# Performance work log

Hardware: AMD Instinct MI355X
Metric: run time of the kernel (lower is better)

The kernel has to match this reference:

```python
import jax, jax.numpy as jnp
import numpy as np

B, T, W, L, H, TW = 2, 4096, 2048, 2048, 8, 4
HD = L // H  # head dim for block-diagonal gate projections


def setup_inputs() -> dict:
    key = jax.random.key(0)
    ks = jax.random.split(key, 16)
    inv_sqrt_w = 1.0 / np.sqrt(W)
    inv_sqrt_l = 1.0 / np.sqrt(L)
    inv_sqrt_hd = 1.0 / np.sqrt(HD)
    return {
        "x": jax.random.normal(ks[0], (B, T, W), dtype=jnp.float32),
        "segment_pos": jnp.tile(jnp.arange(T, dtype=jnp.int32), (B, 1)),
        # linear_y, linear_x: width -> lru_width
        "w_y": jax.random.normal(ks[1], (W, L), dtype=jnp.float32) * inv_sqrt_w,
        "b_y": jnp.zeros((L,), dtype=jnp.float32),
        "w_x": jax.random.normal(ks[2], (W, L), dtype=jnp.float32) * inv_sqrt_w,
        "b_x": jnp.zeros((L,), dtype=jnp.float32),
        # linear_out: lru_width -> width
        "w_out": jax.random.normal(ks[3], (L, W), dtype=jnp.float32) * inv_sqrt_l,
        "b_out": jnp.zeros((W,), dtype=jnp.float32),
        # depthwise causal temporal conv, kernel [TW, L]
        "conv_w": jax.random.normal(ks[4], (TW, L), dtype=jnp.float32) / np.sqrt(TW),
        "conv_b": jnp.zeros((L,), dtype=jnp.float32),
        # RG-LRU: a_param and two block-diagonal gate projections
        "a_param": jax.random.uniform(ks[5], (L,), dtype=jnp.float32, minval=-2.0, maxval=1.0),
        "igate_w": jax.random.normal(ks[6], (H, HD, HD), dtype=jnp.float32) * inv_sqrt_hd,
        "igate_b": jnp.zeros((H, HD), dtype=jnp.float32),
        "agate_w": jax.random.normal(ks[7], (H, HD, HD), dtype=jnp.float32) * inv_sqrt_hd,
        "agate_b": jnp.zeros((H, HD), dtype=jnp.float32),
    }


def _block_diag_linear(u, w, b):
    # u: [B,T,L] -> [B,T,H,HD] blockwise projected -> [B,T,L]
    uh = u.reshape(u.shape[0], u.shape[1], H, HD)
    y = jnp.einsum("bthd,hde->bthe", uh, w) + b
    return y.reshape(u.shape)


def _forward(x, segment_pos, w_y, b_y, w_x, b_x, w_out, b_out,
             conv_w, conv_b, a_param, igate_w, igate_b, agate_w, agate_b):
    # gate branch: linear_y + tanh-approx GELU
    y = jax.nn.gelu(jnp.einsum("btw,wl->btl", x, w_y) + b_y, approximate=True)
    # recurrent branch: linear_x
    xb = jnp.einsum("btw,wl->btl", x, w_x) + b_x
    # causal depthwise temporal conv (width TW), zero history before t=0
    x_pad = jnp.pad(xb, ((0, 0), (TW - 1, 0), (0, 0)))
    conv = conv_b + sum(conv_w[j] * x_pad[:, j:j + T] for j in range(TW))
    # RG-LRU gates
    gate_x = jax.nn.sigmoid(_block_diag_linear(conv, igate_w, igate_b))
    gate_a = jax.nn.sigmoid(_block_diag_linear(conv, agate_w, agate_b))
    log_a = -8.0 * gate_a * jax.nn.softplus(a_param)  # [B,T,L]
    a = jnp.exp(log_a)
    reset = (segment_pos == 0)[..., None]  # [B,T,1]
    multiplier = jnp.sqrt(1.0 - jnp.exp(2.0 * log_a))
    multiplier = jnp.where(reset, 1.0, multiplier)
    normed = conv * gate_x * multiplier
    a_masked = jnp.where(reset, 0.0, a)
    # diagonal linear recurrence: h_t = a_t * h_{t-1} + normed_t
    def step(h, inp):
        a_t, x_t = inp
        h = a_t * h + x_t
        return h, h
    h0 = jnp.zeros((x.shape[0], L), dtype=x.dtype)
    _, hs = jax.lax.scan(step, h0, (a_masked.transpose(1, 0, 2), normed.transpose(1, 0, 2)))
    hs = hs.transpose(1, 0, 2)  # [B,T,L]
    # elementwise gate then output projection
    return jnp.einsum("btl,lw->btw", hs * y, w_out) + b_out


def reference(x, segment_pos, w_y, b_y, w_x, b_x, w_out, b_out,
              conv_w, conv_b, a_param, igate_w, igate_b, agate_w, agate_b):
    return _forward(x, segment_pos, w_y, b_y, w_x, b_x, w_out, b_out,
                    conv_w, conv_b, a_param, igate_w, igate_b, agate_w, agate_b)
```

## Files before the change

### kernel.cpp

```cpp
#include <hip/hip_runtime.h>
#include <cstdint>
#include <math.h>

typedef _Float16 f16;
typedef f16 f16x8 __attribute__((ext_vector_type(8)));
typedef f16 f16x4 __attribute__((ext_vector_type(4)));
typedef float f32x4 __attribute__((ext_vector_type(4)));

#define BATCH 2
#define TSEQ 4096
#define WID 2048
#define LRU 2048
#define NHEAD 8
#define HDIM 256
#define MTOT (BATCH * TSEQ)
#define CT 128
#define NC (TSEQ / CT)

__device__ __forceinline__ void gl2lds16(const f16* g, f16* l) {
  __builtin_amdgcn_global_load_lds(
      (__attribute__((address_space(1))) uint32_t*)(uintptr_t)g,
      (__attribute__((address_space(3))) uint32_t*)(uint32_t)(uintptr_t)l,
      16, 0, 0);
}

__device__ __forceinline__ float sigmoidf_(float x) { return 1.f / (1.f + expf(-x)); }
__device__ __forceinline__ float f16bits_to_f(uint32_t b) {
  return (float)__builtin_bit_cast(f16, (uint16_t)b);
}

__global__ void prep_kernel(const float* __restrict__ x, f16* __restrict__ Xh,
                            const float* __restrict__ w_y, const float* __restrict__ w_x,
                            const float* __restrict__ w_out,
                            f16* __restrict__ wyT, f16* __restrict__ wxT, f16* __restrict__ woutT,
                            const float* __restrict__ ig, const float* __restrict__ ag,
                            f16* __restrict__ igT, f16* __restrict__ agT) {
  __shared__ float tile[32][33];
  const int bid = blockIdx.x, t = threadIdx.x;
  if (bid < 16384) {
    int i = bid * 256 + t;
    float4 v = ((const float4*)x)[i];
    f16x4 o = { (f16)v.x, (f16)v.y, (f16)v.z, (f16)v.w };
    ((f16x4*)Xh)[i] = o;
    return;
  }
  const int tx = t & 31, ty = t >> 5;
  const float* ib; f16* ob; int R, C, c0, r0;
  if (bid < 28672) {
    int idx = bid - 16384;
    int z = idx >> 12, tl = idx & 4095;
    ib = z == 0 ? w_y : (z == 1 ? w_x : w_out);
    ob = z == 0 ? wyT : (z == 1 ? wxT : woutT);
    R = 2048; C = 2048;
    c0 = (tl & 63) * 32; r0 = (tl >> 6) * 32;
  } else {
    int idx = bid - 28672;
    int z = idx >> 6, tl = idx & 63;
    ib = (z < 8 ? ig : ag) + (long long)(z & 7) * HDIM * HDIM;
    ob = (z < 8 ? igT : agT) + (long long)(z & 7) * HDIM * HDIM;
    R = HDIM; C = HDIM;
    c0 = (tl & 7) * 32; r0 = (tl >> 3) * 32;
  }
#pragma unroll
  for (int i = 0; i < 32; i += 8)
    tile[ty + i][tx] = ib[(long long)(r0 + ty + i) * C + c0 + tx];
  __syncthreads();
#pragma unroll
  for (int i = 0; i < 32; i += 8)
    ob[(long long)(c0 + ty + i) * R + r0 + tx] = (f16)tile[tx][ty + i];
}

__global__ __launch_bounds__(256, 2) void gemm_dual(
    const f16* __restrict__ A, const f16* __restrict__ B1T, const f16* __restrict__ B2T,
    const float* __restrict__ b1, const float* __restrict__ b2,
    f16* __restrict__ Y, f16* __restrict__ X2, int M, int N, int K) {
  __shared__ __align__(16) f16 As[3][128 * 32];
  __shared__ __align__(16) f16 B1s[3][128 * 32];
  __shared__ __align__(16) f16 B2s[3][128 * 32];
  const int m0 = blockIdx.x * 128, n0 = blockIdx.y * 128;
  const int t = threadIdx.x;
  const int lane = t & 63, wave = t >> 6;
  const int wr = (wave >> 1) * 64, wc = (wave & 1) * 64;
  const int l15 = lane & 15, quad = lane >> 4;
  const int srow = t >> 2;
  const int scol = ((t & 3) ^ ((srow >> 1) & 3)) * 8;
  const int sl = (quad ^ ((l15 >> 1) & 3)) * 8;

  const f16* Ag = A + (long long)(m0 + srow) * K + scol;
  const f16* B1g = B1T + (long long)(n0 + srow) * K + scol;
  const f16* B2g = B2T + (long long)(n0 + srow) * K + scol;
  const long long h64 = (long long)64 * K;

  auto STAGE = [&](int tt, int bb) {
    const f16* a = Ag + tt * 32;
    const f16* p1 = B1g + tt * 32;
    const f16* p2 = B2g + tt * 32;
    gl2lds16(a, &As[bb][t * 8]);    gl2lds16(a + h64, &As[bb][64 * 32 + t * 8]);
    gl2lds16(p1, &B1s[bb][t * 8]);  gl2lds16(p1 + h64, &B1s[bb][64 * 32 + t * 8]);
    gl2lds16(p2, &B2s[bb][t * 8]);  gl2lds16(p2 + h64, &B2s[bb][64 * 32 + t * 8]);
  };

  f32x4 c1[4][4] = {};
  f32x4 c2[4][4] = {};
  const int NT = K >> 5;
  STAGE(0, 0); STAGE(1, 1);
  asm volatile("s_waitcnt vmcnt(6)" ::: "memory");
  __builtin_amdgcn_s_barrier();
  __builtin_amdgcn_sched_barrier(0);
  int bufc = 0, bufs = 2;
  for (int tt = 0; tt < NT; ++tt) {
    if (tt + 2 < NT) STAGE(tt + 2, bufs);
    f16x8 af[4], b1f[4], b2f[4];
#pragma unroll
    for (int i = 0; i < 4; ++i)
      af[i] = *(const f16x8*)&As[bufc][(wr + i * 16 + l15) * 32 + sl];
#pragma unroll
    for (int j = 0; j < 4; ++j) {
      b1f[j] = *(const f16x8*)&B1s[bufc][(wc + j * 16 + l15) * 32 + sl];
      b2f[j] = *(const f16x8*)&B2s[bufc][(wc + j * 16 + l15) * 32 + sl];
    }
    __builtin_amdgcn_s_setprio(1);
#pragma unroll
    for (int i = 0; i < 4; ++i)
#pragma unroll
      for (int j = 0; j < 4; ++j) {
        c1[i][j] = __builtin_amdgcn_mfma_f32_16x16x32_f16(af[i], b1f[j], c1[i][j], 0, 0, 0);
        c2[i][j] = __builtin_amdgcn_mfma_f32_16x16x32_f16(af[i], b2f[j], c2[i][j], 0, 0, 0);
      }
    __builtin_amdgcn_s_setprio(0);
    if (tt + 1 < NT) {
      if (tt + 2 < NT) { asm volatile("s_waitcnt vmcnt(6)" ::: "memory"); }
      else             { asm volatile("s_waitcnt vmcnt(0)" ::: "memory"); }
      __builtin_amdgcn_s_barrier();
      __builtin_amdgcn_sched_barrier(0);
    }
    bufc = (bufc + 1 == 3) ? 0 : bufc + 1;
    bufs = (bufs + 1 == 3) ? 0 : bufs + 1;
  }
#pragma unroll
  for (int i = 0; i < 4; ++i) {
#pragma unroll
    for (int j = 0; j < 4; ++j) {
      const int col = n0 + wc + j * 16 + l15;
      const float b1v = b1[col], b2v = b2[col];
      const int row0 = m0 + wr + i * 16 + quad * 4;
#pragma unroll
      for (int r = 0; r < 4; ++r) {
        long long off = (long long)(row0 + r) * N + col;
        float v = c1[i][j][r] + b1v;
        float u = v + 0.044715f * v * v * v;
        float g = 0.5f * v * (1.f + tanhf(0.7978845608028654f * u));
        Y[off] = (f16)g;
        X2[off] = (f16)(c2[i][j][r] + b2v);
      }
    }
  }
}

__global__ __launch_bounds__(256, 2) void gemm_bt(
    const f16* __restrict__ A, const f16* __restrict__ BT, const float* __restrict__ bias,
    float* __restrict__ Cf, int M, int N, int K) {
  __shared__ __align__(16) f16 As[3][128 * 32];
  __shared__ __align__(16) f16 Bs[3][128 * 32];
  const int m0 = blockIdx.x * 128, n0 = blockIdx.y * 128;
  const int t = threadIdx.x;
  const int lane = t & 63, wave = t >> 6;
  const int wr = (wave >> 1) * 64, wc = (wave & 1) * 64;
  const int l15 = lane & 15, quad = lane >> 4;
  const int srow = t >> 2;
  const int scol = ((t & 3) ^ ((srow >> 1) & 3)) * 8;
  const int sl = (quad ^ ((l15 >> 1) & 3)) * 8;

  const f16* Ag = A + (long long)(m0 + srow) * K + scol;
  const f16* Bg = BT + (long long)(n0 + srow) * K + scol;
  const long long h64 = (long long)64 * K;

  auto STAGE = [&](int tt, int bb) {
    const f16* a = Ag + tt * 32;
    const f16* p = Bg + tt * 32;
    gl2lds16(a, &As[bb][t * 8]); gl2lds16(a + h64, &As[bb][64 * 32 + t * 8]);
    gl2lds16(p, &Bs[bb][t * 8]); gl2lds16(p + h64, &Bs[bb][64 * 32 + t * 8]);
  };

  f32x4 acc[4][4] = {};
  const int NT = K >> 5;
  STAGE(0, 0); STAGE(1, 1);
  asm volatile("s_waitcnt vmcnt(4)" ::: "memory");
  __builtin_amdgcn_s_barrier();
  __builtin_amdgcn_sched_barrier(0);
  int bufc = 0, bufs = 2;
  for (int tt = 0; tt < NT; ++tt) {
    if (tt + 2 < NT) STAGE(tt + 2, bufs);
    f16x8 af[4], bf[4];
#pragma unroll
    for (int i = 0; i < 4; ++i)
      af[i] = *(const f16x8*)&As[bufc][(wr + i * 16 + l15) * 32 + sl];
#pragma unroll
    for (int j = 0; j < 4; ++j)
      bf[j] = *(const f16x8*)&Bs[bufc][(wc + j * 16 + l15) * 32 + sl];
    __builtin_amdgcn_s_setprio(1);
#pragma unroll
    for (int i = 0; i < 4; ++i)
#pragma unroll
      for (int j = 0; j < 4; ++j)
        acc[i][j] = __builtin_amdgcn_mfma_f32_16x16x32_f16(af[i], bf[j], acc[i][j], 0, 0, 0);
    __builtin_amdgcn_s_setprio(0);
    if (tt + 1 < NT) {
      if (tt + 2 < NT) { asm volatile("s_waitcnt vmcnt(4)" ::: "memory"); }
      else             { asm volatile("s_waitcnt vmcnt(0)" ::: "memory"); }
      __builtin_amdgcn_s_barrier();
      __builtin_amdgcn_sched_barrier(0);
    }
    bufc = (bufc + 1 == 3) ? 0 : bufc + 1;
    bufs = (bufs + 1 == 3) ? 0 : bufs + 1;
  }
#pragma unroll
  for (int i = 0; i < 4; ++i) {
#pragma unroll
    for (int j = 0; j < 4; ++j) {
      const int col = n0 + wc + j * 16 + l15;
      const float bv = bias[col];
      const int row0 = m0 + wr + i * 16 + quad * 4;
#pragma unroll
      for (int r = 0; r < 4; ++r)
        Cf[(long long)(row0 + r) * N + col] = acc[i][j][r] + bv;
    }
  }
}

__global__ __launch_bounds__(256, 2) void gates_fused(
    const f16* __restrict__ XBh, const float* __restrict__ cw, const float* __restrict__ cb,
    const f16* __restrict__ BiT, const f16* __restrict__ BaT,
    const float* __restrict__ ib, const float* __restrict__ ab,
    const float* __restrict__ a_param, const int* __restrict__ segpos,
    uint32_t* __restrict__ AN, float* __restrict__ Ac, float* __restrict__ Hc) {
  __shared__ __align__(16) f16 As[128 * 256];
  __shared__ __align__(16) f16 Bi[128 * 32];
  __shared__ __align__(16) f16 Ba[128 * 32];
  const int m0 = blockIdx.x * 128;
  const int h = blockIdx.y >> 1;
  const int half = blockIdx.y & 1;
  const int ncol0 = h * HDIM + half * 128;
  const int t = threadIdx.x;
  const int lane = t & 63, wave = t >> 6;
  const int wr = (wave >> 1) * 64, wc = (wave & 1) * 64;
  const int l15 = lane & 15, quad = lane >> 4;

#pragma unroll 4
  for (int it = 0; it < 16; ++it) {
    int idx = it * 256 + t;
    int r = idx >> 5, kc = idx & 31;
    int m = m0 + r, tpos = m & (TSEQ - 1);
    int colbase = h * HDIM + kc * 8;
    float acc[8];
    {
      float4 c0 = *(const float4*)&cb[colbase];
      float4 c1 = *(const float4*)&cb[colbase + 4];
      acc[0] = c0.x; acc[1] = c0.y; acc[2] = c0.z; acc[3] = c0.w;
      acc[4] = c1.x; acc[5] = c1.y; acc[6] = c1.z; acc[7] = c1.w;
    }
#pragma unroll
    for (int d = 0; d < 4; ++d) {
      if (tpos >= d) {
        f16x8 xv = *(const f16x8*)&XBh[(long long)(m - d) * LRU + colbase];
        float4 w0 = *(const float4*)&cw[(3 - d) * LRU + colbase];
        float4 w1 = *(const float4*)&cw[(3 - d) * LRU + colbase + 4];
        acc[0] += w0.x * (float)xv[0]; acc[1] += w0.y * (float)xv[1];
        acc[2] += w0.z * (float)xv[2]; acc[3] += w0.w * (float)xv[3];
        acc[4] += w1.x * (float)xv[4]; acc[5] += w1.y * (float)xv[5];
        acc[6] += w1.z * (float)xv[6]; acc[7] += w1.w * (float)xv[7];
      }
    }
    f16x8 o;
#pragma unroll
    for (int k = 0; k < 8; ++k) o[k] = (f16)acc[k];
    int gs = (kc & ~7) | ((kc ^ r) & 7);
    *(f16x8*)&As[r * 256 + gs * 8] = o;
  }
  __syncthreads();

  const int srow = t >> 2, scol = (t & 3) * 8;
  const f16* Big = BiT + (long long)(ncol0 + srow) * HDIM + scol;
  const f16* Bag = BaT + (long long)(ncol0 + srow) * HDIM + scol;
  f32x4 ci[4][4] = {};
  f32x4 ca[4][4] = {};
  for (int k0 = 0; k0 < HDIM; k0 += 32) {
    gl2lds16(Big, &Bi[t * 8]); gl2lds16(Big + 64 * HDIM, &Bi[64 * 32 + t * 8]);
    gl2lds16(Bag, &Ba[t * 8]); gl2lds16(Bag + 64 * HDIM, &Ba[64 * 32 + t * 8]);
    Big += 32; Bag += 32;
    __syncthreads();
    f16x8 af[4], bif[4], baf[4];
#pragma unroll
    for (int i = 0; i < 4; ++i) {
      int row = wr + i * 16 + l15;
      int g = (k0 >> 3) + quad;
      int gsw = (g & ~7) | ((g ^ row) & 7);
      af[i] = *(const f16x8*)&As[row * 256 + gsw * 8];
    }
#pragma unroll
    for (int j = 0; j < 4; ++j) {
      bif[j] = *(const f16x8*)&Bi[(wc + j * 16 + l15) * 32 + quad * 8];
      baf[j] = *(const f16x8*)&Ba[(wc + j * 16 + l15) * 32 + quad * 8];
    }
#pragma unroll
    for (int i = 0; i < 4; ++i)
#pragma unroll
      for (int j = 0; j < 4; ++j) {
        ci[i][j] = __builtin_amdgcn_mfma_f32_16x16x32_f16(af[i], bif[j], ci[i][j], 0, 0, 0);
        ca[i][j] = __builtin_amdgcn_mfma_f32_16x16x32_f16(af[i], baf[j], ca[i][j], 0, 0, 0);
      }
    __syncthreads();
  }

  const int mb = m0 >> 12;
  const int cch = (m0 & (TSEQ - 1)) >> 7;
  float Aw[4], hw[4];
#pragma unroll
  for (int j = 0; j < 4; ++j) {
    const int cl = wc + j * 16 + l15;
    const int col = ncol0 + cl;
    const float ibv = ib[col], abv = ab[col];
    const float sp = log1pf(expf(a_param[col]));
    float A4[4], h4[4];
#pragma unroll
    for (int i = 0; i < 4; ++i) {
      float Aseg = 1.f, hseg = 0.f;
#pragma unroll
      for (int r = 0; r < 4; ++r) {
        const int rowL = wr + i * 16 + quad * 4 + r;
        const int row = m0 + rowL;
        float gx = sigmoidf_(ci[i][j][r] + ibv);
        float ga = sigmoidf_(ca[i][j][r] + abv);
        float la = -8.f * ga * sp;
        bool rs = (segpos[row] == 0);
        float a = rs ? 0.f : expf(la);
        uint32_t afx = __float2uint_rn(a * 65536.f);
        if (afx > 65535u) afx = 65535u;
        float aq = (float)afx * (1.f / 65536.f);
        int cfull = half * 128 + cl;
        int g = cfull >> 3, e = cfull & 7;
        int gsw = (g & ~7) | ((g ^ rowL) & 7);
        float cv = (float)As[rowL * 256 + gsw * 8 + e];
        float mult = rs ? 1.f : sqrtf(fmaxf(1.f - aq * aq, 0.f));
        f16 nh = (f16)(cv * gx * mult);
        AN[(long long)row * LRU + col] =
            afx | ((uint32_t)__builtin_bit_cast(uint16_t, nh) << 16);
        float xq = (float)nh;
        hseg = aq * hseg + xq;
        Aseg *= aq;
      }
      A4[i] = Aseg; h4[i] = hseg;
    }
#pragma unroll
    for (int i = 0; i < 4; ++i) {
      float A = A4[i], hv = h4[i];
#pragma unroll
      for (int d = 1; d <= 2; d <<= 1) {
        int src = quad >= d ? lane - 16 * d : lane;
        float Ap = __shfl(A, src);
        float hp = __shfl(hv, src);
        if (quad >= d) { hv = A * hp + hv; A = Ap * A; }
      }
      A4[i] = __shfl(A, 48 + l15);
      h4[i] = __shfl(hv, 48 + l15);
    }
    float Awv = 1.f, hwv = 0.f;
#pragma unroll
    for (int i = 0; i < 4; ++i) { hwv = A4[i] * hwv + h4[i]; Awv *= A4[i]; }
    Aw[j] = Awv; hw[j] = hwv;
  }
  float* carry = (float*)Bi;
  __syncthreads();
  if (wr == 0 && quad == 0) {
#pragma unroll
    for (int j = 0; j < 4; ++j) {
      int cl = wc + j * 16 + l15;
      carry[cl * 2] = Aw[j]; carry[cl * 2 + 1] = hw[j];
    }
  }
  __syncthreads();
  if (wr == 64 && quad == 0) {
#pragma unroll
    for (int j = 0; j < 4; ++j) {
      int cl = wc + j * 16 + l15;
      float At = carry[cl * 2], ht = carry[cl * 2 + 1];
      float A = At * Aw[j];
      float hv = Aw[j] * ht + hw[j];
      int o = (mb * NC + cch) * LRU + ncol0 + cl;
      Ac[o] = A; Hc[o] = hv;
    }
  }
}

__global__ void scan23_kernel(const uint32_t* __restrict__ AN,
                              const float* __restrict__ Ac, const float* __restrict__ Hc,
                              const f16* __restrict__ Yh, f16* __restrict__ G) {
  int l = blockIdx.x * 256 + threadIdx.x;
  int c = blockIdx.y, b = blockIdx.z;
  float hv = 0.f;
  for (int cc = 0; cc < c; ++cc) {
    int o = (b * NC + cc) * LRU + l;
    hv = Ac[o] * hv + Hc[o];
  }
  long long base = ((long long)b * TSEQ + (long long)c * CT) * LRU + l;
#pragma unroll 4
  for (int s = 0; s < CT; ++s) {
    long long o = base + (long long)s * LRU;
    uint32_t p = AN[o];
    float a = (float)(p & 0xFFFFu) * (1.f / 65536.f);
    float x = f16bits_to_f(p >> 16);
    hv = a * hv + x;
    G[o] = (f16)(hv * (float)Yh[o]);
  }
}

extern "C" void kernel_launch(void* const* d_in, const int* in_sizes, int n_in,
                              void* d_out, int out_size, void* d_ws, size_t ws_size,
                              hipStream_t stream) {
  (void)in_sizes; (void)n_in; (void)out_size; (void)ws_size;
  const float* x          = (const float*)d_in[0];
  const int*   segment_pos= (const int*)d_in[1];
  const float* w_y        = (const float*)d_in[2];
  const float* b_y        = (const float*)d_in[3];
  const float* w_x        = (const float*)d_in[4];
  const float* b_x        = (const float*)d_in[5];
  const float* w_out      = (const float*)d_in[6];
  const float* b_out      = (const float*)d_in[7];
  const float* conv_w     = (const float*)d_in[8];
  const float* conv_b     = (const float*)d_in[9];
  const float* a_param    = (const float*)d_in[10];
  const float* igate_w    = (const float*)d_in[11];
  const float* igate_b    = (const float*)d_in[12];
  const float* agate_w    = (const float*)d_in[13];
  const float* agate_b    = (const float*)d_in[14];
  float* out = (float*)d_out;

  char* base = (char*)d_ws;
  size_t off = 0;
  auto alloc = [&](size_t nbytes) -> void* {
    void* p = base + off;
    off = (off + nbytes + 255) & ~(size_t)255;
    return p;
  };
  f16*     Xh    = (f16*)alloc((size_t)MTOT * LRU * 2);
  f16*     Yh    = (f16*)alloc((size_t)MTOT * LRU * 2);
  f16*     XBh   = (f16*)alloc((size_t)MTOT * LRU * 2);
  uint32_t* AN   = (uint32_t*)alloc((size_t)MTOT * LRU * 4);
  f16*     wyT   = (f16*)alloc((size_t)WID * LRU * 2);
  f16*     wxT   = (f16*)alloc((size_t)WID * LRU * 2);
  f16*     woutT = (f16*)alloc((size_t)LRU * WID * 2);
  f16*     igwT  = (f16*)alloc((size_t)NHEAD * HDIM * HDIM * 2);
  f16*     agwT  = (f16*)alloc((size_t)NHEAD * HDIM * HDIM * 2);
  float*   Ac    = (float*)alloc((size_t)BATCH * NC * LRU * 4);
  float*   Hc    = (float*)alloc((size_t)BATCH * NC * LRU * 4);
  f16*     G     = Xh;

  prep_kernel<<<29696, 256, 0, stream>>>(x, Xh, w_y, w_x, w_out, wyT, wxT, woutT,
                                         igate_w, agate_w, igwT, agwT);
  gemm_dual<<<dim3(MTOT / 128, LRU / 128), 256, 0, stream>>>(
      Xh, wyT, wxT, b_y, b_x, Yh, XBh, MTOT, LRU, WID);
  gates_fused<<<dim3(MTOT / 128, 2 * NHEAD), 256, 0, stream>>>(
      XBh, conv_w, conv_b, igwT, agwT, igate_b, agate_b, a_param, segment_pos, AN, Ac, Hc);
  scan23_kernel<<<dim3(LRU / 256, NC, BATCH), 256, 0, stream>>>(AN, Ac, Hc, Yh, G);
  gemm_bt<<<dim3(MTOT / 128, WID / 128), 256, 0, stream>>>(G, woutT, b_out, out, MTOT, WID, LRU);
}
```

Baseline: 558.2 us.

## Replace 128x128 GEMMs with templated 256x256 tile GEMM using split-phase pipeline

Replaces the dual-output GEMM and the output GEMM with one templated 256x256-tile kernel run on 512 threads, with 8 waves each computing 128x64. The main loop is split into two MFMA phases, with LDS fragment loads and global-to-LDS staging of A and B interleaved between extra barriers. The larger tile is meant to raise arithmetic intensity and cut global traffic per FLOP. The cost is that the fused gate/x GEMM becomes two launches that each reread X, and the extra barriers add synchronisation. LDS use is 96KB per block, which may limit occupancy below the requested 2 blocks per CU.

```diff
diff --git a/kernel.cpp b/kernel.cpp
--- a/kernel.cpp
+++ b/kernel.cpp
@@ -70,160 +70,110 @@
     ob[(long long)(c0 + ty + i) * R + r0 + tx] = (f16)tile[tx][ty + i];
 }
 
-__global__ __launch_bounds__(256, 2) void gemm_dual(
-    const f16* __restrict__ A, const f16* __restrict__ B1T, const f16* __restrict__ B2T,
-    const float* __restrict__ b1, const float* __restrict__ b2,
-    f16* __restrict__ Y, f16* __restrict__ X2, int M, int N, int K) {
-  __shared__ __align__(16) f16 As[3][128 * 32];
-  __shared__ __align__(16) f16 B1s[3][128 * 32];
-  __shared__ __align__(16) f16 B2s[3][128 * 32];
-  const int m0 = blockIdx.x * 128, n0 = blockIdx.y * 128;
+template <int MODE>
+__global__ __launch_bounds__(512, 2) void gemm_256(
+    const f16* __restrict__ A, const f16* __restrict__ BT,
+    const float* __restrict__ bias, void* __restrict__ Cout,
+    int M, int N, int K) {
+  __shared__ __align__(16) f16 As[3][256 * 32];
+  __shared__ __align__(16) f16 Bs[3][256 * 32];
+  const int m0 = blockIdx.x * 256, n0 = blockIdx.y * 256;
   const int t = threadIdx.x;
   const int lane = t & 63, wave = t >> 6;
-  const int wr = (wave >> 1) * 64, wc = (wave & 1) * 64;
+  const int wr = (wave >> 2) * 128;
+  const int wc = (wave & 3) * 64;
   const int l15 = lane & 15, quad = lane >> 4;
   const int srow = t >> 2;
-  const int scol = ((t & 3) ^ ((srow >> 1) & 3)) * 8;
+  const int sg = ((t & 3) ^ ((srow >> 1) & 3)) * 8;
   const int sl = (quad ^ ((l15 >> 1) & 3)) * 8;
 
-  const f16* Ag = A + (long long)(m0 + srow) * K + scol;
-  const f16* B1g = B1T + (long long)(n0 + srow) * K + scol;
-  const f16* B2g = B2T + (long long)(n0 + srow) * K + scol;
-  const long long h64 = (long long)64 * K;
-
-  auto STAGE = [&](int tt, int bb) {
+  const f16* Ag = A + (long long)(m0 + srow) * K + sg;
+  const f16* Bg = BT + (long long)(n0 + srow) * K + sg;
+  const long long h128 = (long long)128 * K;
+
+  auto STAGE_A = [&](int tt, int bb) {
     const f16* a = Ag + tt * 32;
-    const f16* p1 = B1g + tt * 32;
-    const f16* p2 = B2g + tt * 32;
-    gl2lds16(a, &As[bb][t * 8]);    gl2lds16(a + h64, &As[bb][64 * 32 + t * 8]);
-    gl2lds16(p1, &B1s[bb][t * 8]);  gl2lds16(p1 + h64, &B1s[bb][64 * 32 + t * 8]);
-    gl2lds16(p2, &B2s[bb][t * 8]);  gl2lds16(p2 + h64, &B2s[bb][64 * 32 + t * 8]);
+    gl2lds16(a, &As[bb][t * 8]);
+    gl2lds16(a + h128, &As[bb][128 * 32 + t * 8]);
   };
-
-  f32x4 c1[4][4] = {};
-  f32x4 c2[4][4] = {};
+  auto STAGE_B = [&](int tt, int bb) {
+    const f16* b = Bg + tt * 32;
+    gl2lds16(b, &Bs[bb][t * 8]);
+    gl2lds16(b + h128, &Bs[bb][128 * 32 + t * 8]);
+  };
+
+  f32x4 c[8][4] = {};
   const int NT = K >> 5;
-  STAGE(0, 0); STAGE(1, 1);
-  asm volatile("s_waitcnt vmcnt(6)" ::: "memory");
-  __builtin_amdgcn_s_barrier();
-  __builtin_amdgcn_sched_barrier(0);
-  int bufc = 0, bufs = 2;
-  for (int tt = 0; tt < NT; ++tt) {
-    if (tt + 2 < NT) STAGE(tt + 2, bufs);
-    f16x8 af[4], b1f[4], b2f[4];
-#pragma unroll
-    for (int i = 0; i < 4; ++i)
-      af[i] = *(const f16x8*)&As[bufc][(wr + i * 16 + l15) * 32 + sl];
-#pragma unroll
-    for (int j = 0; j < 4; ++j) {
-      b1f[j] = *(const f16x8*)&B1s[bufc][(wc + j * 16 + l15) * 32 + sl];
-      b2f[j] = *(const f16x8*)&B2s[bufc][(wc + j * 16 + l15) * 32 + sl];
-    }
-    __builtin_amdgcn_s_setprio(1);
-#pragma unroll
-    for (int i = 0; i < 4; ++i)
-#pragma unroll
-      for (int j = 0; j < 4; ++j) {
-        c1[i][j] = __builtin_amdgcn_mfma_f32_16x16x32_f16(af[i], b1f[j], c1[i][j], 0, 0, 0);
-        c2[i][j] = __builtin_amdgcn_mfma_f32_16x16x32_f16(af[i], b2f[j], c2[i][j], 0, 0, 0);
-      }
-    __builtin_amdgcn_s_setprio(0);
-    if (tt + 1 < NT) {
-      if (tt + 2 < NT) { asm volatile("s_waitcnt vmcnt(6)" ::: "memory"); }
-      else             { asm volatile("s_waitcnt vmcnt(0)" ::: "memory"); }
-      __builtin_amdgcn_s_barrier();
-      __builtin_amdgcn_sched_barrier(0);
-    }
-    bufc = (bufc + 1 == 3) ? 0 : bufc + 1;
-    bufs = (bufs + 1 == 3) ? 0 : bufs + 1;
-  }
-#pragma unroll
-  for (int i = 0; i < 4; ++i) {
-#pragma unroll
-    for (int j = 0; j < 4; ++j) {
-      const int col = n0 + wc + j * 16 + l15;
-      const float b1v = b1[col], b2v = b2[col];
-      const int row0 = m0 + wr + i * 16 + quad * 4;
-#pragma unroll
-      for (int r = 0; r < 4; ++r) {
-        long long off = (long long)(row0 + r) * N + col;
-        float v = c1[i][j][r] + b1v;
-        float u = v + 0.044715f * v * v * v;
-        float g = 0.5f * v * (1.f + tanhf(0.7978845608028654f * u));
-        Y[off] = (f16)g;
-        X2[off] = (f16)(c2[i][j][r] + b2v);
-      }
-    }
-  }
-}
-
-__global__ __launch_bounds__(256, 2) void gemm_bt(
-    const f16* __restrict__ A, const f16* __restrict__ BT, const float* __restrict__ bias,
-    float* __restrict__ Cf, int M, int N, int K) {
-  __shared__ __align__(16) f16 As[3][128 * 32];
-  __shared__ __align__(16) f16 Bs[3][128 * 32];
-  const int m0 = blockIdx.x * 128, n0 = blockIdx.y * 128;
-  const int t = threadIdx.x;
-  const int lane = t & 63, wave = t >> 6;
-  const int wr = (wave >> 1) * 64, wc = (wave & 1) * 64;
-  const int l15 = lane & 15, quad = lane >> 4;
-  const int srow = t >> 2;
-  const int scol = ((t & 3) ^ ((srow >> 1) & 3)) * 8;
-  const int sl = (quad ^ ((l15 >> 1) & 3)) * 8;
-
-  const f16* Ag = A + (long long)(m0 + srow) * K + scol;
-  const f16* Bg = BT + (long long)(n0 + srow) * K + scol;
-  const long long h64 = (long long)64 * K;
-
-  auto STAGE = [&](int tt, int bb) {
-    const f16* a = Ag + tt * 32;
-    const f16* p = Bg + tt * 32;
-    gl2lds16(a, &As[bb][t * 8]); gl2lds16(a + h64, &As[bb][64 * 32 + t * 8]);
-    gl2lds16(p, &Bs[bb][t * 8]); gl2lds16(p + h64, &Bs[bb][64 * 32 + t * 8]);
-  };
-
-  f32x4 acc[4][4] = {};
-  const int NT = K >> 5;
-  STAGE(0, 0); STAGE(1, 1);
+  STAGE_A(0, 0); STAGE_B(0, 0); STAGE_A(1, 1); STAGE_B(1, 1);
   asm volatile("s_waitcnt vmcnt(4)" ::: "memory");
   __builtin_amdgcn_s_barrier();
   __builtin_amdgcn_sched_barrier(0);
   int bufc = 0, bufs = 2;
   for (int tt = 0; tt < NT; ++tt) {
-    if (tt + 2 < NT) STAGE(tt + 2, bufs);
-    f16x8 af[4], bf[4];
+    const f16* asrc = &As[bufc][0];
+    const f16* bsrc = &Bs[bufc][0];
+    f16x8 af[8], bf[4];
 #pragma unroll
     for (int i = 0; i < 4; ++i)
-      af[i] = *(const f16x8*)&As[bufc][(wr + i * 16 + l15) * 32 + sl];
+      af[i] = *(const f16x8*)&asrc[(wr + i * 16 + l15) * 32 + sl];
 #pragma unroll
     for (int j = 0; j < 4; ++j)
-      bf[j] = *(const f16x8*)&Bs[bufc][(wc + j * 16 + l15) * 32 + sl];
+      bf[j] = *(const f16x8*)&bsrc[(wc + j * 16 + l15) * 32 + sl];
+    if (tt + 2 < NT) STAGE_A(tt + 2, bufs);
+    __builtin_amdgcn_s_barrier();
+    asm volatile("s_waitcnt lgkmcnt(0)" ::: "memory");
+    __builtin_amdgcn_sched_barrier(0);
     __builtin_amdgcn_s_setprio(1);
 #pragma unroll
     for (int i = 0; i < 4; ++i)
 #pragma unroll
       for (int j = 0; j < 4; ++j)
-        acc[i][j] = __builtin_amdgcn_mfma_f32_16x16x32_f16(af[i], bf[j], acc[i][j], 0, 0, 0);
+        c[i][j] = __builtin_amdgcn_mfma_f32_16x16x32_f16(af[i], bf[j], c[i][j], 0, 0, 0);
     __builtin_amdgcn_s_setprio(0);
+    __builtin_amdgcn_s_barrier();
+#pragma unroll
+    for (int i = 4; i < 8; ++i)
+      af[i] = *(const f16x8*)&asrc[(wr + i * 16 + l15) * 32 + sl];
+    if (tt + 2 < NT) STAGE_B(tt + 2, bufs);
     if (tt + 1 < NT) {
       if (tt + 2 < NT) { asm volatile("s_waitcnt vmcnt(4)" ::: "memory"); }
       else             { asm volatile("s_waitcnt vmcnt(0)" ::: "memory"); }
-      __builtin_amdgcn_s_barrier();
-      __builtin_amdgcn_sched_barrier(0);
-    }
+    }
+    __builtin_amdgcn_s_barrier();
+    asm volatile("s_waitcnt lgkmcnt(0)" ::: "memory");
+    __builtin_amdgcn_sched_barrier(0);
+    __builtin_amdgcn_s_setprio(1);
+#pragma unroll
+    for (int i = 4; i < 8; ++i)
+#pragma unroll
+      for (int j = 0; j < 4; ++j)
+        c[i][j] = __builtin_amdgcn_mfma_f32_16x16x32_f16(af[i], bf[j], c[i][j], 0, 0, 0);
+    __builtin_amdgcn_s_setprio(0);
+    __builtin_amdgcn_s_barrier();
     bufc = (bufc + 1 == 3) ? 0 : bufc + 1;
     bufs = (bufs + 1 == 3) ? 0 : bufs + 1;
   }
 #pragma unroll
-  for (int i = 0; i < 4; ++i) {
+  for (int i = 0; i < 8; ++i) {
 #pragma unroll
     for (int j = 0; j < 4; ++j) {
       const int col = n0 + wc + j * 16 + l15;
       const float bv = bias[col];
       const int row0 = m0 + wr + i * 16 + quad * 4;
 #pragma unroll
-      for (int r = 0; r < 4; ++r)
-        Cf[(long long)(row0 + r) * N + col] = acc[i][j][r] + bv;
+      for (int r = 0; r < 4; ++r) {
+        float v = c[i][j][r] + bv;
+        long long off = (long long)(row0 + r) * N + col;
+        if constexpr (MODE == 0) {
+          float u = v + 0.044715f * v * v * v;
+          float g = 0.5f * v * (1.f + tanhf(0.7978845608028654f * u));
+          ((f16*)Cout)[off] = (f16)g;
+        } else if constexpr (MODE == 1) {
+          ((f16*)Cout)[off] = (f16)v;
+        } else {
+          ((float*)Cout)[off] = v;
+        }
+      }
     }
   }
 }
@@ -457,10 +407,13 @@
 
   prep_kernel<<<29696, 256, 0, stream>>>(x, Xh, w_y, w_x, w_out, wyT, wxT, woutT,
                                          igate_w, agate_w, igwT, agwT);
-  gemm_dual<<<dim3(MTOT / 128, LRU / 128), 256, 0, stream>>>(
-      Xh, wyT, wxT, b_y, b_x, Yh, XBh, MTOT, LRU, WID);
+  gemm_256<0><<<dim3(MTOT / 256, LRU / 256), 512, 0, stream>>>(
+      Xh, wyT, b_y, Yh, MTOT, LRU, WID);
+  gemm_256<1><<<dim3(MTOT / 256, LRU / 256), 512, 0, stream>>>(
+      Xh, wxT, b_x, XBh, MTOT, LRU, WID);
   gates_fused<<<dim3(MTOT / 128, 2 * NHEAD), 256, 0, stream>>>(
       XBh, conv_w, conv_b, igwT, agwT, igate_b, agate_b, a_param, segment_pos, AN, Ac, Hc);
   scan23_kernel<<<dim3(LRU / 256, NC, BATCH), 256, 0, stream>>>(AN, Ac, Hc, Yh, G);
-  gemm_bt<<<dim3(MTOT / 128, WID / 128), 256, 0, stream>>>(G, woutT, b_out, out, MTOT, WID, LRU);
-}
+  gemm_256<2><<<dim3(MTOT / 256, WID / 256), 512, 0, stream>>>(
+      G, woutT, b_out, out, MTOT, WID, LRU);
+}
```

Measured after the change: 546.8 us. -2.0%, faster.
